# Optimization experiments

Measured on AMD Instinct MI355X. Metric: run time of the kernel, lower is better.

## Reference

```python
import jax, jax.numpy as jnp
import numpy as np

B, T, C = 4, 2048, 1024
H = 16
D = C // H  # head_dim = 64


def setup_inputs() -> dict:
    key = jax.random.key(0)
    k1, k2, k3 = jax.random.split(key, 3)
    x = jax.random.normal(k1, (B, T, C), dtype=jnp.float32)
    # torch nn.Linear weight layout: [out_features, in_features]; y = x @ W.T
    w_attn = jax.random.normal(k2, (3 * C, C), dtype=jnp.float32) * (1.0 / np.sqrt(C))
    w_proj = jax.random.normal(k3, (C, C), dtype=jnp.float32) * (1.0 / np.sqrt(C))
    return {"x": x, "w_attn": w_attn, "w_proj": w_proj}


def _attention(x, w_attn, w_proj):
    qkv = jnp.einsum('btc,fc->btf', x, w_attn)           # [B,T,3C]
    q, k, v = jnp.split(qkv, 3, axis=-1)
    # [B,T,C] -> [B,H,T,D]
    q = q.reshape(B, T, H, D).transpose(0, 2, 1, 3)
    k = k.reshape(B, T, H, D).transpose(0, 2, 1, 3)
    v = v.reshape(B, T, H, D).transpose(0, 2, 1, 3)
    att = jnp.einsum('bhqd,bhkd->bhqk', q, k) * (1.0 / np.sqrt(D))
    causal = jnp.tril(jnp.ones((T, T), dtype=bool))      # [T,T]
    att = jnp.where(causal[None, None], att, -jnp.inf)
    att = jax.nn.softmax(att, axis=-1)
    out = jnp.einsum('bhqk,bhkd->bhqd', att, v)          # [B,H,T,D]
    out = out.transpose(0, 2, 1, 3).reshape(B, T, C)
    return jnp.einsum('btc,fc->btf', out, w_proj)        # [B,T,C]


def reference(x, w_attn, w_proj):
    return _attention(x, w_attn, w_proj)
```

## Files before the change

kernel.cpp:

```cpp
#include <hip/hip_runtime.h>
#include <hip/hip_bf16.h>

typedef __attribute__((ext_vector_type(8))) short s8b;
typedef __attribute__((ext_vector_type(4))) float f4;
typedef unsigned short u16;

union U8 { s8b v; unsigned long long u[2]; };

__device__ __forceinline__ u16 f2bf(float f) {
  union { float f; unsigned u; } x; x.f = f;
  unsigned r = x.u + 0x7fffu + ((x.u >> 16) & 1u);
  return (u16)(r >> 16);
}

__device__ __forceinline__ float exp2a(float x) {
  float r;
  asm("v_exp_f32 %0, %1" : "=v"(r) : "v"(x));
  return r;
}

__device__ __forceinline__ void gload16(const void* g, void* l) {
  __builtin_amdgcn_global_load_lds(
      (const __attribute__((address_space(1))) void*)g,
      (__attribute__((address_space(3))) void*)l, 16, 0, 0);
}

__global__ void cvt3_kernel(const float* __restrict__ x, const float* __restrict__ wa,
                            const float* __restrict__ wp, u16* __restrict__ xb,
                            u16* __restrict__ wab, u16* __restrict__ wpb) {
  const int base = blockIdx.x * blockDim.x + threadIdx.x;
#pragma unroll
  for (int rep = 0; rep < 2; ++rep) {
    const int i = base + rep * 1572864;
    const float4* src;
    ushort4* dst;
    int idx;
    if (i < 2097152) { src = (const float4*)x; dst = (ushort4*)xb; idx = i; }
    else if (i < 2883584) { src = (const float4*)wa; dst = (ushort4*)wab; idx = i - 2097152; }
    else { src = (const float4*)wp; dst = (ushort4*)wpb; idx = i - 2883584; }
    const float4 v = src[idx];
    ushort4 o;
    o.x = f2bf(v.x); o.y = f2bf(v.y); o.z = f2bf(v.z); o.w = f2bf(v.w);
    dst[idx] = o;
  }
}

#define BMT 128
#define BNT 128
#define BKT 64

template<int MODE, int TILES>
__global__ __launch_bounds__(256, 2)
void gemm_bt(const u16* __restrict__ A, const u16* __restrict__ Bm,
             float* __restrict__ Cf,
             u16* __restrict__ qo, u16* __restrict__ ko, u16* __restrict__ vo,
             int N, int K, int GX) {
  __shared__ u16 lds[2][2][BMT * BKT];
  const int tid = threadIdx.x;
  const int lane = tid & 63;
  const int w = tid >> 6;
  const int wr = w >> 1, wc = w & 1;
  const int ric = lane >> 3;
  const int ssw = (lane & 7) ^ ric;

  auto tile_ptrs = [&](int t, const u16*& Ab, const u16*& Bb, int& bm, int& bn) {
    const int d = blockIdx.x + t * gridDim.x;
    const int xcd = d & 7, ib = d >> 3;
    bm = xcd * 8 + (ib & 7);
    bn = ib >> 3;
    Ab = A + (size_t)bm * BMT * K;
    Bb = Bm + (size_t)bn * BNT * K;
  };

  const int nk = K / BKT;
  const u16 *Ab, *Bb, *AbN, *BbN;
  int bm, bn, bmN, bnN;
  tile_ptrs(0, Ab, Bb, bm, bn);

  {
#pragma unroll
    for (int c = 0; c < 4; ++c) {
      const int rch = w * 32 + c * 8;
      gload16(Ab + (size_t)(rch + ric) * K + ssw * 8, &lds[0][0][rch * BKT]);
      gload16(Bb + (size_t)(rch + ric) * K + ssw * 8, &lds[0][1][rch * BKT]);
    }
  }
  __syncthreads();

  for (int t = 0; t < TILES; ++t) {
    if (t + 1 < TILES) tile_ptrs(t + 1, AbN, BbN, bmN, bnN);
    f4 acc[4][4] = {};

    for (int kt = 0; kt < nk; kt += 2) {
#pragma unroll
      for (int h = 0; h < 2; ++h) {
        const int ktg = kt + h;
        {
          const u16* sA;
          const u16* sB;
          int ko_;
          bool do_stage = true;
          if (ktg + 1 < nk) { sA = Ab; sB = Bb; ko_ = (ktg + 1) * BKT; }
          else if (t + 1 < TILES) { sA = AbN; sB = BbN; ko_ = 0; }
          else do_stage = false;
          if (do_stage) {
#pragma unroll
            for (int c = 0; c < 4; ++c) {
              const int rch = w * 32 + c * 8;
              gload16(sA + (size_t)(rch + ric) * K + ko_ + ssw * 8, &lds[h ^ 1][0][rch * BKT]);
              gload16(sB + (size_t)(rch + ric) * K + ko_ + ssw * 8, &lds[h ^ 1][1][rch * BKT]);
            }
          }
        }
        const u16* At = &lds[h][0][0];
        const u16* Bt = &lds[h][1][0];
#pragma unroll
        for (int kk = 0; kk < 2; ++kk) {
          s8b a[4], b[4];
#pragma unroll
          for (int m = 0; m < 4; ++m) {
            const int row = wr * 64 + m * 16 + (lane & 15);
            a[m] = *(const s8b*)(At + row * BKT + ((((kk << 2) + (lane >> 4)) ^ (row & 7)) << 3));
          }
#pragma unroll
          for (int n = 0; n < 4; ++n) {
            const int row = wc * 64 + n * 16 + (lane & 15);
            b[n] = *(const s8b*)(Bt + row * BKT + ((((kk << 2) + (lane >> 4)) ^ (row & 7)) << 3));
          }
#pragma unroll
          for (int m = 0; m < 4; ++m)
#pragma unroll
            for (int n = 0; n < 4; ++n)
              acc[m][n] = __builtin_amdgcn_mfma_f32_16x16x32_bf16(a[m], b[n], acc[m][n], 0, 0, 0);
        }
        __syncthreads();
      }
    }

    if (MODE == 0) {
#pragma unroll
      for (int n = 0; n < 4; ++n) {
        const int f = bn * BNT + wc * 64 + n * 16 + (lane & 15);
        const int which = f >> 10;
        const int rem = f & 1023;
        const int h = rem >> 6, dd = rem & 63;
        if (which == 2) {
#pragma unroll
          for (int m = 0; m < 4; ++m) {
            const int i0 = bm * BMT + wr * 64 + m * 16 + (lane >> 4) * 4;
            const int bb = i0 >> 11, t0 = i0 & 2047;
            ushort4 pk;
            pk.x = f2bf(acc[m][n][0]);
            pk.y = f2bf(acc[m][n][1]);
            pk.z = f2bf(acc[m][n][2]);
            pk.w = f2bf(acc[m][n][3]);
            *(ushort4*)(&vo[((size_t)((bb << 4) + h) * 64 + dd) * 2048 + t0]) = pk;
          }
        } else {
          u16* dst = which == 0 ? qo : ko;
          const float sc = which == 0 ? 0.18033688f : 1.0f;
#pragma unroll
          for (int m = 0; m < 4; ++m) {
#pragma unroll
            for (int j = 0; j < 4; ++j) {
              const int i = bm * BMT + wr * 64 + m * 16 + (lane >> 4) * 4 + j;
              const int bb = i >> 11, tt = i & 2047;
              dst[((size_t)((bb << 4) + h) * 2048 + tt) * 64 + dd] = f2bf(acc[m][n][j] * sc);
            }
          }
        }
      }
    } else {
#pragma unroll
      for (int m = 0; m < 4; ++m) {
#pragma unroll
        for (int j = 0; j < 4; ++j) {
          const int i = bm * BMT + wr * 64 + m * 16 + (lane >> 4) * 4 + j;
#pragma unroll
          for (int n = 0; n < 4; ++n) {
            const int f = bn * BNT + wc * 64 + n * 16 + (lane & 15);
            Cf[(size_t)i * N + f] = acc[m][n][j];
          }
        }
      }
    }

    Ab = AbN; Bb = BbN; bm = bmN; bn = bnN;
  }
}

__global__ __launch_bounds__(256, 3)
void attn_kernel(const u16* __restrict__ q, const u16* __restrict__ k,
                 const u16* __restrict__ vt, u16* __restrict__ ao) {
  __shared__ u16 Kl[64 * 64];
  __shared__ u16 VTl[64 * 64];
  __shared__ u16 Pl[4][16 * 64];
  const int tid = threadIdx.x, lane = tid & 63, w = tid >> 6;
  const int dd = blockIdx.x;
  const int xcd = dd & 7, ib = dd >> 3;
  const int bh = xcd * 8 + (ib & 7);
  const int j4 = ib >> 3;
  const int s4 = j4 >> 2, r4 = j4 & 3;
  const int qi = (s4 == 0) ? 15 - r4 : (s4 == 1) ? 8 + r4 : (s4 == 2) ? 7 - r4 : r4;
  const int b = bh >> 4, h16 = bh & 15;
  const size_t hb = (size_t)bh * 2048 * 64;
  const int qlo = lane & 15, hi = lane >> 4;
  const int r0 = tid >> 3, sl = tid & 7;
  u16* pw = &Pl[w][0];

  const s8b ones = {16256, 16256, 16256, 16256, 16256, 16256, 16256, 16256};

  const u16* kp = k + hb + (size_t)r0 * 64 + sl * 8;
  const u16* vp = vt + hb + (size_t)r0 * 2048 + sl * 8;
  s8b kr[2], vr[2];
  auto load_regs = [&]() {
    kr[0] = *(const s8b*)kp;
    kr[1] = *(const s8b*)(kp + 32 * 64);
    vr[0] = *(const s8b*)vp;
    vr[1] = *(const s8b*)(vp + 32 * 2048);
    kp += 64 * 64;
    vp += 64;
  };
  auto write_lds = [&]() {
#pragma unroll
    for (int c0 = 0; c0 < 2; ++c0) {
      const int r = r0 + c0 * 32;
      const int off = r * 64 + ((sl ^ (r & 7) ^ (r >> 3)) << 3);
      *(s8b*)(&Kl[off]) = kr[c0];
      *(s8b*)(&VTl[off]) = vr[c0];
    }
  };

  auto softpack = [&](f4 (&s)[4], U8 (&pf)[2]) {
#pragma unroll
    for (int n = 0; n < 4; ++n)
#pragma unroll
      for (int j = 0; j < 4; ++j) s[n][j] = exp2a(s[n][j]);
#pragma unroll
    for (int n = 0; n < 4; ++n) {
      __hip_bfloat162 h0 = __float22bfloat162_rn(make_float2(s[n][0], s[n][1]));
      __hip_bfloat162 h1 = __float22bfloat162_rn(make_float2(s[n][2], s[n][3]));
      unsigned lo, hi2;
      __builtin_memcpy(&lo, &h0, 4);
      __builtin_memcpy(&hi2, &h1, 4);
      const unsigned long long w64 =
          (unsigned long long)lo | ((unsigned long long)hi2 << 32);
      const int cw = ((n << 2) + hi) ^ qlo;
      *(unsigned long long*)(pw + (qlo << 6) + (cw << 2)) = w64;
    }
#pragma unroll
    for (int kk = 0; kk < 2; ++kk) {
      const int ca = ((kk << 3) + (hi << 1)) ^ qlo;
      pf[kk].u[0] = *(const unsigned long long*)(pw + (qlo << 6) + (ca << 2));
      pf[kk].u[1] = *(const unsigned long long*)(pw + (qlo << 6) + ((ca ^ 1) << 2));
    }
  };

  const int nkt = 2 * qi + 2;
  s8b qf[2][2];
#pragma unroll
  for (int g = 0; g < 2; ++g) {
    const u16* qp = q + hb + (size_t)(qi * 128 + w * 32 + g * 16 + qlo) * 64 + hi * 8;
    qf[g][0] = *(const s8b*)qp;
    qf[g][1] = *(const s8b*)(qp + 32);
  }
  f4 acc0[5] = {}, acc1[5] = {};

  load_regs();
  write_lds();
  __syncthreads();

  for (int kt = 0; kt < nkt; ++kt) {
    const bool pf_next = (kt + 1 < nkt);
    if (pf_next) load_regs();

    f4 s0[4], s1[4];
#pragma unroll
    for (int n = 0; n < 4; ++n) {
      s0[n] = (f4){-64.f, -64.f, -64.f, -64.f};
      s1[n] = (f4){-64.f, -64.f, -64.f, -64.f};
    }
    __builtin_amdgcn_s_setprio(1);
#pragma unroll
    for (int n = 0; n < 4; ++n) {
      const int row = n * 16 + qlo;
      const int swz = (row & 7) ^ (row >> 3);
#pragma unroll
      for (int kk = 0; kk < 2; ++kk) {
        const s8b kf = *(const s8b*)(&Kl[row * 64 + ((((kk << 2) + hi) ^ swz) << 3)]);
        s0[n] = __builtin_amdgcn_mfma_f32_16x16x32_bf16(kf, qf[0][kk], s0[n], 0, 0, 0);
        s1[n] = __builtin_amdgcn_mfma_f32_16x16x32_bf16(kf, qf[1][kk], s1[n], 0, 0, 0);
      }
    }
    __builtin_amdgcn_s_setprio(0);

    const int dmb = (2 * qi - kt) * 64;
    if (dmb < 64) {
      const int thr0 = w * 32 + qlo + dmb;
      const int thr1 = thr0 + 16;
#pragma unroll
      for (int n = 0; n < 4; ++n)
#pragma unroll
        for (int j = 0; j < 4; ++j) {
          const int kidx = n * 16 + hi * 4 + j;
          if (kidx > thr0) s0[n][j] = -1e30f;
          if (kidx > thr1) s1[n][j] = -1e30f;
        }
    }

    U8 pf0[2], pf1[2];
    softpack(s0, pf0);
    softpack(s1, pf1);

    __builtin_amdgcn_s_setprio(1);
#pragma unroll
    for (int dn = 0; dn < 4; ++dn) {
      const int vrow = dn * 16 + qlo;
      const int vswz = (vrow & 7) ^ (vrow >> 3);
#pragma unroll
      for (int kk = 0; kk < 2; ++kk) {
        const s8b vf = *(const s8b*)(&VTl[vrow * 64 + ((((kk << 2) + hi) ^ vswz) << 3)]);
        acc0[dn] = __builtin_amdgcn_mfma_f32_16x16x32_bf16(pf0[kk].v, vf, acc0[dn], 0, 0, 0);
        acc1[dn] = __builtin_amdgcn_mfma_f32_16x16x32_bf16(pf1[kk].v, vf, acc1[dn], 0, 0, 0);
      }
    }
#pragma unroll
    for (int kk = 0; kk < 2; ++kk) {
      acc0[4] = __builtin_amdgcn_mfma_f32_16x16x32_bf16(pf0[kk].v, ones, acc0[4], 0, 0, 0);
      acc1[4] = __builtin_amdgcn_mfma_f32_16x16x32_bf16(pf1[kk].v, ones, acc1[4], 0, 0, 0);
    }
    __builtin_amdgcn_s_setprio(0);

    __syncthreads();
    if (pf_next) {
      write_lds();
      __syncthreads();
    }
  }

#pragma unroll
  for (int g = 0; g < 2; ++g) {
    const f4* accg = g ? acc1 : acc0;
#pragma unroll
    for (int j = 0; j < 4; ++j) {
      const float rl = 1.0f / accg[4][j];
      const int t = qi * 128 + w * 32 + g * 16 + hi * 4 + j;
#pragma unroll
      for (int dn = 0; dn < 4; ++dn) {
        const int dcol = dn * 16 + qlo;
        ao[((size_t)(b * 2048 + t)) * 1024 + h16 * 64 + dcol] = f2bf(accg[dn][j] * rl);
      }
    }
  }
}

extern "C" void kernel_launch(void* const* d_in, const int* in_sizes, int n_in,
                              void* d_out, int out_size, void* d_ws, size_t ws_size,
                              hipStream_t stream) {
  const float* x = (const float*)d_in[0];
  const float* w_attn = (const float*)d_in[1];
  const float* w_proj = (const float*)d_in[2];
  float* out = (float*)d_out;
  char* ws = (char*)d_ws;

  u16* xb  = (u16*)(ws);
  u16* wab = (u16*)(ws + (16u << 20));
  u16* wpb = (u16*)(ws + (22u << 20));
  u16* qb  = (u16*)(ws + (24u << 20));
  u16* kb  = (u16*)(ws + (40u << 20));
  u16* vb  = (u16*)(ws + (56u << 20));
  u16* ao  = xb;

  cvt3_kernel<<<6144, 256, 0, stream>>>(x, w_attn, w_proj, xb, wab, wpb);

  gemm_bt<0, 3><<<512, 256, 0, stream>>>(xb, wab, nullptr, qb, kb, vb,
                                         3072, 1024, 24);
  attn_kernel<<<1024, 256, 0, stream>>>(qb, kb, vb, ao);
  gemm_bt<1, 1><<<512, 256, 0, stream>>>(ao, wpb, out, nullptr, nullptr, nullptr,
                                         1024, 1024, 8);
}
```

Baseline: 137.4 us.

## Replace persistent double-buffered QKV GEMM with single-buffered one-tile-per-block kernel

Adds a new gemm_sb kernel that computes one 128x128 output tile per block with a single LDS buffer. It stages each K-slice, syncs, computes, syncs again, then loads the next slice. It replaces the persistent 3-tiles-per-block, double-buffered gemm_bt launch for the QKV projection with a 1536-block grid. The aim is to halve LDS use so more blocks fit per CU and to drop the persistent-loop overhead, giving up overlap of global loads with MFMA compute.

```diff
diff --git a/kernel.cpp b/kernel.cpp
--- a/kernel.cpp
+++ b/kernel.cpp
@@ -48,6 +48,120 @@
 #define BMT 128
 #define BNT 128
 #define BKT 64
+
+template<int MODE>
+__global__ __launch_bounds__(256, 2)
+void gemm_sb(const u16* __restrict__ A, const u16* __restrict__ Bm,
+             float* __restrict__ Cf,
+             u16* __restrict__ qo, u16* __restrict__ ko, u16* __restrict__ vo,
+             int N, int K) {
+  __shared__ u16 lds[2][BMT * BKT];
+  const int tid = threadIdx.x;
+  const int lane = tid & 63;
+  const int w = tid >> 6;
+  const int wr = w >> 1, wc = w & 1;
+  const int ric = lane >> 3;
+  const int ssw = (lane & 7) ^ ric;
+
+  const int d = blockIdx.x;
+  const int xcd = d & 7, ib = d >> 3;
+  const int bm = xcd * 8 + (ib & 7);
+  const int bn = ib >> 3;
+  const u16* Ab = A + (size_t)bm * BMT * K;
+  const u16* Bb = Bm + (size_t)bn * BNT * K;
+
+  auto stage = [&](int kt) {
+    const int ko_ = kt * BKT;
+#pragma unroll
+    for (int c = 0; c < 4; ++c) {
+      const int rch = w * 32 + c * 8;
+      gload16(Ab + (size_t)(rch + ric) * K + ko_ + ssw * 8, &lds[0][rch * BKT]);
+      gload16(Bb + (size_t)(rch + ric) * K + ko_ + ssw * 8, &lds[1][rch * BKT]);
+    }
+  };
+
+  const int nk = K / BKT;
+  f4 acc[4][4] = {};
+  stage(0);
+  __syncthreads();
+
+  for (int kt = 0; kt < nk; ++kt) {
+    const u16* At = &lds[0][0];
+    const u16* Bt = &lds[1][0];
+#pragma unroll
+    for (int kk = 0; kk < 2; ++kk) {
+      s8b a[4], b[4];
+#pragma unroll
+      for (int m = 0; m < 4; ++m) {
+        const int row = wr * 64 + m * 16 + (lane & 15);
+        a[m] = *(const s8b*)(At + row * BKT + ((((kk << 2) + (lane >> 4)) ^ (row & 7)) << 3));
+      }
+#pragma unroll
+      for (int n = 0; n < 4; ++n) {
+        const int row = wc * 64 + n * 16 + (lane & 15);
+        b[n] = *(const s8b*)(Bt + row * BKT + ((((kk << 2) + (lane >> 4)) ^ (row & 7)) << 3));
+      }
+#pragma unroll
+      for (int m = 0; m < 4; ++m)
+#pragma unroll
+        for (int n = 0; n < 4; ++n)
+          acc[m][n] = __builtin_amdgcn_mfma_f32_16x16x32_bf16(a[m], b[n], acc[m][n], 0, 0, 0);
+    }
+    __syncthreads();
+    if (kt + 1 < nk) {
+      stage(kt + 1);
+      __syncthreads();
+    }
+  }
+
+  if (MODE == 0) {
+#pragma unroll
+    for (int n = 0; n < 4; ++n) {
+      const int f = bn * BNT + wc * 64 + n * 16 + (lane & 15);
+      const int which = f >> 10;
+      const int rem = f & 1023;
+      const int h = rem >> 6, dd = rem & 63;
+      if (which == 2) {
+#pragma unroll
+        for (int m = 0; m < 4; ++m) {
+          const int i0 = bm * BMT + wr * 64 + m * 16 + (lane >> 4) * 4;
+          const int bb = i0 >> 11, t0 = i0 & 2047;
+          ushort4 pk;
+          pk.x = f2bf(acc[m][n][0]);
+          pk.y = f2bf(acc[m][n][1]);
+          pk.z = f2bf(acc[m][n][2]);
+          pk.w = f2bf(acc[m][n][3]);
+          *(ushort4*)(&vo[((size_t)((bb << 4) + h) * 64 + dd) * 2048 + t0]) = pk;
+        }
+      } else {
+        u16* dst = which == 0 ? qo : ko;
+        const float sc = which == 0 ? 0.18033688f : 1.0f;
+#pragma unroll
+        for (int m = 0; m < 4; ++m) {
+#pragma unroll
+          for (int j = 0; j < 4; ++j) {
+            const int i = bm * BMT + wr * 64 + m * 16 + (lane >> 4) * 4 + j;
+            const int bb = i >> 11, tt = i & 2047;
+            dst[((size_t)((bb << 4) + h) * 2048 + tt) * 64 + dd] = f2bf(acc[m][n][j] * sc);
+          }
+        }
+      }
+    }
+  } else {
+#pragma unroll
+    for (int m = 0; m < 4; ++m) {
+#pragma unroll
+      for (int j = 0; j < 4; ++j) {
+        const int i = bm * BMT + wr * 64 + m * 16 + (lane >> 4) * 4 + j;
+#pragma unroll
+        for (int n = 0; n < 4; ++n) {
+          const int f = bn * BNT + wc * 64 + n * 16 + (lane & 15);
+          Cf[(size_t)i * N + f] = acc[m][n][j];
+        }
+      }
+    }
+  }
+}
 
 template<int MODE, int TILES>
 __global__ __launch_bounds__(256, 2)
@@ -373,8 +487,8 @@
 
   cvt3_kernel<<<6144, 256, 0, stream>>>(x, w_attn, w_proj, xb, wab, wpb);
 
-  gemm_bt<0, 3><<<512, 256, 0, stream>>>(xb, wab, nullptr, qb, kb, vb,
-                                         3072, 1024, 24);
+  gemm_sb<0><<<1536, 256, 0, stream>>>(xb, wab, nullptr, qb, kb, vb,
+                                       3072, 1024);
   attn_kernel<<<1024, 256, 0, stream>>>(qb, kb, vb, ao);
   gemm_bt<1, 1><<<512, 256, 0, stream>>>(ao, wpb, out, nullptr, nullptr, nullptr,
                                          1024, 1024, 8);
```

After: 135.4 us. No clear change (-1.5%).
